# Kernel tuning notes

Hardware: AMD Instinct MI355X
Metric: run time of the kernel (lower is better)

The kernel has to match this reference:

```python
import jax, jax.numpy as jnp
import numpy as np

B, S, D, H = 2, 2048, 1024, 16
DH = D // H  # 64


def setup_inputs() -> dict:
    key = jax.random.key(0)
    ks = jax.random.split(key, 12)
    scale = 0.02
    q = jax.random.normal(ks[0], (B, S, D), dtype=jnp.float32)
    k = jax.random.normal(ks[1], (B, S, D), dtype=jnp.float32)
    v = jax.random.normal(ks[2], (B, S, D), dtype=jnp.float32)
    # CTRL-style causal mask: 1.0 above the diagonal (positions to mask), 0.0 elsewhere
    mask = jnp.triu(jnp.ones((S, S), dtype=jnp.float32), k=1)
    Wq = jax.random.normal(ks[3], (D, D), dtype=jnp.float32) * scale
    bq = jnp.zeros((D,), dtype=jnp.float32)
    Wk = jax.random.normal(ks[4], (D, D), dtype=jnp.float32) * scale
    bk = jnp.zeros((D,), dtype=jnp.float32)
    Wv = jax.random.normal(ks[5], (D, D), dtype=jnp.float32) * scale
    bv = jnp.zeros((D,), dtype=jnp.float32)
    Wo = jax.random.normal(ks[6], (D, D), dtype=jnp.float32) * scale
    bo = jnp.zeros((D,), dtype=jnp.float32)
    return {"q": q, "k": k, "v": v, "mask": mask,
            "Wq": Wq, "bq": bq, "Wk": Wk, "bk": bk,
            "Wv": Wv, "bv": bv, "Wo": Wo, "bo": bo}


def _split_heads(x):
    # [B, S, D] -> [B, H, S, DH]
    b, s, _ = x.shape
    return x.reshape(b, s, H, DH).transpose(0, 2, 1, 3)


def reference(q, k, v, mask, Wq, bq, Wk, bk, Wv, bv, Wo, bo):
    # QKV projections
    qh = _split_heads(q @ Wq + bq)  # [B, H, S, DH]
    kh = _split_heads(k @ Wk + bk)
    vh = _split_heads(v @ Wv + bv)
    # scaled dot-product attention with CTRL mask convention (mask * -1e4 added)
    scores = jnp.einsum('bhqd,bhkd->bhqk', qh, kh) / jnp.sqrt(jnp.float32(DH))
    scores = scores + mask * -10000.0  # mask broadcasts [S,S] -> [B,H,S,S]
    weights = jax.nn.softmax(scores, axis=-1)
    ctx = jnp.einsum('bhqk,bhkd->bhqd', weights, vh)  # [B, H, S, DH]
    ctx = ctx.transpose(0, 2, 1, 3).reshape(q.shape[0], -1, D)  # [B, S, D]
    return ctx @ Wo + bo
```

## Files before the change

kernel.cpp:

```cpp
#include <hip/hip_runtime.h>
#include <stdint.h>

typedef unsigned short u16;
typedef __attribute__((ext_vector_type(8))) short bf16x8;
typedef __attribute__((ext_vector_type(4))) float f32x4;
typedef __attribute__((ext_vector_type(4))) unsigned short u16x4;

#define C_SCALE 0.1803368801111204f
#define C_MASK  -14426.950408889634f

__device__ __forceinline__ float bf2f(u16 x) {
  union { uint32_t u; float f; } v; v.u = ((uint32_t)x) << 16; return v.f;
}
__device__ __forceinline__ u16 f2bf(float f) {
  union { float f; uint32_t u; } v; v.f = f;
  return (u16)((v.u + 0x7FFFu + ((v.u >> 16) & 1u)) >> 16);
}

__device__ __forceinline__ void load_lds16(const void* g, void* l) {
  __builtin_amdgcn_global_load_lds(
      (const __attribute__((address_space(1))) uint32_t*)g,
      (__attribute__((address_space(3))) uint32_t*)l, 16, 0, 0);
}

__device__ __forceinline__ uint32_t pack_trunc(uint32_t f_even, uint32_t f_odd) {
  return __builtin_amdgcn_perm(f_odd, f_even, 0x07060302u);
}

__device__ __forceinline__ bool detect_bf16(const u16* __restrict__ q) {
  int lane = threadIdx.x & 63;
  u16 w = q[lane * 4];
  int e = (w >> 7) & 0xFF;
  unsigned long long b = __ballot(e >= 96 && e <= 159);
  return __popcll(b) >= 48;
}

__global__ __launch_bounds__(256) void prep_all(const u16* __restrict__ W0,
                                                const u16* __restrict__ W1,
                                                const u16* __restrict__ W2,
                                                const u16* __restrict__ W3,
                                                u16* __restrict__ WTb,
                                                const u16* __restrict__ q,
                                                const u16* __restrict__ k,
                                                const u16* __restrict__ v,
                                                u16* __restrict__ Acast,
                                                int docast) {
  constexpr int D = 1024;
  const int z = blockIdx.z;
  const bool isbf = detect_bf16(q);

  if (z >= 4) {
    if (!docast || isbf) return;
    const int zi = z - 4;
    const u16* src = zi == 0 ? q : (zi == 1 ? k : v);
    const uint32_t* S = (const uint32_t*)src;
    u16* dst = Acast + (size_t)zi * 4 * 1024 * 1024;
    const int fb = blockIdx.y * 16 + blockIdx.x;
    const int t = threadIdx.x;
#pragma unroll
    for (int it = 0; it < 8; ++it) {
      size_t base = (size_t)fb * 16384 + it * 2048 + t * 8;
      uint4 a = *(const uint4*)&S[base];
      uint4 b = *(const uint4*)&S[base + 4];
      uint4 o;
      o.x = pack_trunc(a.x, a.y); o.y = pack_trunc(a.z, a.w);
      o.z = pack_trunc(b.x, b.y); o.w = pack_trunc(b.z, b.w);
      *(uint4*)&dst[base] = o;
    }
    return;
  }

  __shared__ u16 tile[64][72];
  const u16* W = z == 0 ? W0 : (z == 1 ? W1 : (z == 2 ? W2 : W3));
  u16* WT = WTb + (size_t)z * D * D;
  const int x0 = blockIdx.x * 64, y0 = blockIdx.y * 64;
  const int t = threadIdx.x;
  const int r = t >> 3;
  const int c8 = (t & 7) << 3;
#pragma unroll
  for (int hh = 0; hh < 2; ++hh) {
    int row = r + hh * 32;
    if (isbf) {
      *(uint4*)&tile[row][c8] = *(const uint4*)&W[(size_t)(y0 + row) * D + x0 + c8];
    } else {
      const float* Wf = (const float*)W;
      float4 f0 = *(const float4*)&Wf[(size_t)(y0 + row) * D + x0 + c8];
      float4 f1 = *(const float4*)&Wf[(size_t)(y0 + row) * D + x0 + c8 + 4];
      u16 tmp[8] = {f2bf(f0.x), f2bf(f0.y), f2bf(f0.z), f2bf(f0.w),
                    f2bf(f1.x), f2bf(f1.y), f2bf(f1.z), f2bf(f1.w)};
      *(uint4*)&tile[row][c8] = *(uint4*)tmp;
    }
  }
  __syncthreads();
#pragma unroll
  for (int hh = 0; hh < 2; ++hh) {
    int row = r + hh * 32;
    u16 tmp[8];
#pragma unroll
    for (int i = 0; i < 8; ++i) tmp[i] = tile[c8 + i][row];
    *(uint4*)&WT[(size_t)(x0 + row) * D + y0 + c8] = *(uint4*)tmp;
  }
}


__device__ __forceinline__ void stage_tile32(const u16* __restrict__ src, int row0,
                                             int k0, u16* dst, int wave, int lane) {
  constexpr int K = 1024;
#pragma unroll
  for (int p = 0; p < 2; ++p) {
    int seg = wave * 2 + p;
    int r = seg * 16 + (lane >> 2);
    int c = lane & 3;
    int cg = c ^ ((r >> 1) & 3);
    load_lds16(&src[(size_t)(row0 + r) * K + k0 + cg * 8], dst + seg * 512);
  }
}

#define FRAG_READS(Ab, Bb)                                                    \
  _Pragma("unroll") for (int i = 0; i < 4; ++i) {                             \
    int r = wm + 16 * i + lr;                                                 \
    af[i] = *(const bf16x8*)&(Ab)[r * 32 + ((quad ^ ((r >> 1) & 3)) * 8)];    \
  }                                                                           \
  _Pragma("unroll") for (int jj = 0; jj < 4; ++jj) {                          \
    int r = wn + 16 * jj + lr;                                                \
    bff[jj] = *(const bf16x8*)&(Bb)[r * 32 + ((quad ^ ((r >> 1) & 3)) * 8)];  \
  }

#define MFMA16()                                                              \
  _Pragma("unroll") for (int i = 0; i < 4; ++i)                               \
  _Pragma("unroll") for (int jj = 0; jj < 4; ++jj)                            \
      acc[i][jj] = __builtin_amdgcn_mfma_f32_16x16x32_bf16(af[i], bff[jj],    \
                                                           acc[i][jj], 0, 0, 0);

__device__ __forceinline__ void kloop2_dma(const u16* __restrict__ A,
                                           const u16* __restrict__ BT,
                                           int m0, int n0, u16* As, u16* Bs,
                                           int wave, int lane, f32x4 (&acc)[4][4]) {
  const int quad = lane >> 4, lr = lane & 15;
  const int wm = (wave & 1) * 64, wn = (wave >> 1) * 64;
  auto stage = [&](int t, int buf) {
    stage_tile32(A, m0, t * 32, As + buf * 4096, wave, lane);
    stage_tile32(BT, n0, t * 32, Bs + buf * 4096, wave, lane);
  };
  stage(0, 0);
  __syncthreads();
#pragma unroll 1
  for (int j = 0; j < 16; ++j) {
    const int t0 = 2 * j;
    {
      stage(t0 + 1, 1);
      bf16x8 af[4], bff[4];
      const u16 *Ab = As, *Bb = Bs;
      FRAG_READS(Ab, Bb)
      MFMA16()
      __syncthreads();
    }
    {
      if (t0 + 2 < 32) stage(t0 + 2, 0);
      bf16x8 af[4], bff[4];
      const u16 *Ab = As + 4096, *Bb = Bs + 4096;
      FRAG_READS(Ab, Bb)
      MFMA16()
      __syncthreads();
    }
  }
}

__device__ __forceinline__ void kloop2_f32(const float* __restrict__ Af,
                                           const u16* __restrict__ BT,
                                           int m0, int n0, u16* As, u16* Bs,
                                           int tid, f32x4 (&acc)[4][4]) {
  constexpr int K = 1024;
  const int wave = tid >> 6, lane = tid & 63;
  const int quad = lane >> 4, lr = lane & 15;
  const int wm = (wave & 1) * 64, wn = (wave >> 1) * 64;
  const int ar = tid >> 1, ah = tid & 1;
  const uint32_t* Au = (const uint32_t*)Af;
  uint4 ra0[4], ra1[4];
  auto loadA = [&](int t, uint4 (&r)[4]) {
    const uint32_t* p = &Au[(size_t)(m0 + ar) * K + t * 32 + ah * 16];
    r[0] = *(const uint4*)(p + 0);
    r[1] = *(const uint4*)(p + 4);
    r[2] = *(const uint4*)(p + 8);
    r[3] = *(const uint4*)(p + 12);
  };
  auto writeA = [&](int buf, uint4 (&rr)[4]) {
    uint4 o0, o1;
    o0.x = pack_trunc(rr[0].x, rr[0].y); o0.y = pack_trunc(rr[0].z, rr[0].w);
    o0.z = pack_trunc(rr[1].x, rr[1].y); o0.w = pack_trunc(rr[1].z, rr[1].w);
    o1.x = pack_trunc(rr[2].x, rr[2].y); o1.y = pack_trunc(rr[2].z, rr[2].w);
    o1.z = pack_trunc(rr[3].x, rr[3].y); o1.w = pack_trunc(rr[3].z, rr[3].w);
    int sw = (ar >> 1) & 3;
    int c0 = (2 * ah) ^ sw, c1 = (2 * ah + 1) ^ sw;
    *(uint4*)&As[buf * 4096 + ar * 32 + c0 * 8] = o0;
    *(uint4*)&As[buf * 4096 + ar * 32 + c1 * 8] = o1;
  };
  auto stageB = [&](int t, int buf) {
    stage_tile32(BT, n0, t * 32, Bs + buf * 4096, wave, lane);
  };
  loadA(0, ra0);
  stageB(0, 0);
  loadA(1, ra1);
  writeA(0, ra0);
  __syncthreads();
#pragma unroll 1
  for (int j = 0; j < 16; ++j) {
    const int t0 = 2 * j;
    {
      stageB(t0 + 1, 1);
      writeA(1, ra1);
      if (t0 + 2 < 32) loadA(t0 + 2, ra0);
      bf16x8 af[4], bff[4];
      const u16 *Ab = As, *Bb = Bs;
      FRAG_READS(Ab, Bb)
      MFMA16()
      __syncthreads();
    }
    {
      if (t0 + 2 < 32) { stageB(t0 + 2, 0); writeA(0, ra0); }
      if (t0 + 3 < 32) loadA(t0 + 3, ra1);
      bf16x8 af[4], bff[4];
      const u16 *Ab = As + 4096, *Bb = Bs + 4096;
      FRAG_READS(Ab, Bb)
      MFMA16()
      __syncthreads();
    }
  }
}

__global__ __launch_bounds__(256, 3) void gemm_qkv_pre(
    const u16* __restrict__ q, const u16* __restrict__ k, const u16* __restrict__ v,
    const u16* __restrict__ Acast, const u16* __restrict__ WTb,
    const u16* __restrict__ b0, const u16* __restrict__ b1, const u16* __restrict__ b2,
    u16* __restrict__ Chb) {
  __shared__ u16 As[2 * 4096];
  __shared__ u16 Bs[2 * 4096];
  const int z = blockIdx.y;
  const bool isbf = detect_bf16(q);
  const u16* Araw = z == 0 ? q : (z == 1 ? k : v);
  const u16* A = isbf ? Araw : Acast + (size_t)z * 4 * 1024 * 1024;
  const u16* bias = z == 0 ? b0 : (z == 1 ? b1 : b2);
  const u16* BT = WTb + (size_t)z * 1024 * 1024;
  u16* C = Chb + (size_t)z * 4 * 1024 * 1024;
  const int tid = threadIdx.x;
  const int wave = tid >> 6, lane = tid & 63;
  const int quad = lane >> 4, lr = lane & 15;
  const int f = blockIdx.x;
  const int n0 = (f >> 5) * 128;
  const int m0 = (f & 31) * 128;
  const int wm = (wave & 1) * 64, wn = (wave >> 1) * 64;

  f32x4 acc[4][4] = {};
  kloop2_dma(A, BT, m0, n0, As, Bs, wave, lane, acc);

#pragma unroll
  for (int i = 0; i < 4; ++i) {
#pragma unroll
    for (int jj = 0; jj < 4; ++jj) {
      int n = n0 + wn + 16 * jj + lr;
      float bv = isbf ? bf2f(bias[n]) : ((const float*)bias)[n];
#pragma unroll
      for (int r = 0; r < 4; ++r) {
        int m = m0 + wm + 16 * i + quad * 4 + r;
        float val = acc[i][jj][r] + bv;
        int b = m >> 11, s = m & 2047, h = n >> 6, dh = n & 63;
        C[((size_t)(b * 16 + h) * 2048 + s) * 64 + dh] = f2bf(val);
      }
    }
  }
}

__global__ __launch_bounds__(256, 3) void gemm_qkv_fb(
    const u16* __restrict__ A0, const u16* __restrict__ A1, const u16* __restrict__ A2,
    const u16* __restrict__ WTb,
    const u16* __restrict__ b0, const u16* __restrict__ b1, const u16* __restrict__ b2,
    u16* __restrict__ Chb) {
  __shared__ u16 As[2 * 4096];
  __shared__ u16 Bs[2 * 4096];
  const int z = blockIdx.y;
  const u16* A = z == 0 ? A0 : (z == 1 ? A1 : A2);
  const u16* bias = z == 0 ? b0 : (z == 1 ? b1 : b2);
  const u16* BT = WTb + (size_t)z * 1024 * 1024;
  u16* C = Chb + (size_t)z * 4 * 1024 * 1024;
  const bool isbf = detect_bf16(A0);
  const int tid = threadIdx.x;
  const int wave = tid >> 6, lane = tid & 63;
  const int quad = lane >> 4, lr = lane & 15;
  const int f = blockIdx.x;
  const int n0 = (f >> 5) * 128;
  const int m0 = (f & 31) * 128;
  const int wm = (wave & 1) * 64, wn = (wave >> 1) * 64;

  f32x4 acc[4][4] = {};
  if (isbf) kloop2_dma(A, BT, m0, n0, As, Bs, wave, lane, acc);
  else      kloop2_f32((const float*)A, BT, m0, n0, As, Bs, tid, acc);

#pragma unroll
  for (int i = 0; i < 4; ++i) {
#pragma unroll
    for (int jj = 0; jj < 4; ++jj) {
      int n = n0 + wn + 16 * jj + lr;
      float bv = isbf ? bf2f(bias[n]) : ((const float*)bias)[n];
#pragma unroll
      for (int r = 0; r < 4; ++r) {
        int m = m0 + wm + 16 * i + quad * 4 + r;
        float val = acc[i][jj][r] + bv;
        int b = m >> 11, s = m & 2047, h = n >> 6, dh = n & 63;
        C[((size_t)(b * 16 + h) * 2048 + s) * 64 + dh] = f2bf(val);
      }
    }
  }
}

__global__ __launch_bounds__(256, 2) void gemm_out(const u16* __restrict__ A,
                                                   const u16* __restrict__ BT,
                                                   const u16* __restrict__ bias,
                                                   u16* __restrict__ C,
                                                   const u16* __restrict__ qprobe) {
  constexpr int N = 1024, K = 1024;
  __shared__ u16 As[2 * 2048];
  __shared__ u16 Bs[2 * 4096];
  const bool isbf = detect_bf16(qprobe);
  const int tid = threadIdx.x;
  const int wave = tid >> 6, lane = tid & 63;
  const int quad = lane >> 4, lr = lane & 15;
  const int f = blockIdx.x;
  const int n0 = (f >> 6) * 128;
  const int m0 = (f & 63) * 64;
  const int wm = (wave & 1) * 32, wn = (wave >> 1) * 64;

  auto stage = [&](int t, int buf) {
    {
      int r = wave * 16 + (lane >> 2);
      int c = lane & 3;
      int cg = c ^ ((r >> 1) & 3);
      load_lds16(&A[(size_t)(m0 + r) * K + t * 32 + cg * 8],
                 As + buf * 2048 + wave * 512);
    }
    stage_tile32(BT, n0, t * 32, Bs + buf * 4096, wave, lane);
  };

  f32x4 acc[2][4] = {};
  stage(0, 0);
  __syncthreads();
#pragma unroll 1
  for (int j = 0; j < 16; ++j) {
    const int t0 = 2 * j;
#pragma unroll
    for (int half = 0; half < 2; ++half) {
      const int t = t0 + half;
      if (t + 1 < 32) stage(t + 1, (t + 1) & 1);
      bf16x8 af[2], bff[4];
      const u16* Ab = As + (t & 1) * 2048;
      const u16* Bb = Bs + (t & 1) * 4096;
#pragma unroll
      for (int i = 0; i < 2; ++i) {
        int r = wm + 16 * i + lr;
        af[i] = *(const bf16x8*)&Ab[r * 32 + ((quad ^ ((r >> 1) & 3)) * 8)];
      }
#pragma unroll
      for (int jj = 0; jj < 4; ++jj) {
        int r = wn + 16 * jj + lr;
        bff[jj] = *(const bf16x8*)&Bb[r * 32 + ((quad ^ ((r >> 1) & 3)) * 8)];
      }
#pragma unroll
      for (int i = 0; i < 2; ++i)
#pragma unroll
        for (int jj = 0; jj < 4; ++jj)
          acc[i][jj] =
              __builtin_amdgcn_mfma_f32_16x16x32_bf16(af[i], bff[jj], acc[i][jj], 0, 0, 0);
      __syncthreads();
    }
  }

#pragma unroll
  for (int i = 0; i < 2; ++i) {
#pragma unroll
    for (int jj = 0; jj < 4; ++jj) {
      int n = n0 + wn + 16 * jj + lr;
      float bv = isbf ? bf2f(bias[n]) : ((const float*)bias)[n];
#pragma unroll
      for (int r = 0; r < 4; ++r) {
        int m = m0 + wm + 16 * i + quad * 4 + r;
        float val = acc[i][jj][r] + bv;
        size_t idx = (size_t)m * N + n;
        if (isbf) C[idx] = f2bf(val);
        else ((float*)C)[idx] = val;
      }
    }
  }
}

__global__ __launch_bounds__(256, 2) void attn_fwd(const u16* __restrict__ Qh,
                                                   const u16* __restrict__ Kh,
                                                   const u16* __restrict__ Vh,
                                                   u16* __restrict__ ctx) {
  constexpr int S = 2048, DH = 64, Dm = 1024;
  __shared__ u16 Ks[2][64 * 64];
  __shared__ u16 Vt[2][64 * 72];
  __shared__ u16 Pl[4][16 * 72];
  const int tid = threadIdx.x;
  const int wave = tid >> 6, lane = tid & 63;
  const int quad = lane >> 4, lr = lane & 15;
  const int bh = blockIdx.y;
  const int bx = (int)blockIdx.x;
  const size_t base = (size_t)bh * S * DH;
  const u16* Q = Qh + base;
  const u16* Kp = Kh + base;
  const u16* Vp = Vh + base;
  u16* Plw = Pl[wave];
  const int b = bh >> 4, h = bh & 15;

  const int vkey2 = (tid & 31) * 2, vd8 = (tid >> 5) * 8;
  uint4 va, vbr;

  auto stageK = [&](int kt, int kbuf) {
#pragma unroll
    for (int p = 0; p < 2; ++p) {
      int s = (wave * 2 + p) * 64 + lane;
      int r = s >> 3, cg = (s & 7) ^ (r & 7);
      load_lds16(&Kp[(size_t)(kt + r) * DH + cg * 8], &Ks[kbuf][(wave * 2 + p) * 512]);
    }
  };
  auto loadV = [&](int kt) {
    va  = *(const uint4*)&Vp[(size_t)(kt + vkey2) * DH + vd8];
    vbr = *(const uint4*)&Vp[(size_t)(kt + vkey2 + 1) * DH + vd8];
  };
  auto writeV = [&](int vbuf) {
    const u16* pa = (const u16*)&va;
    const u16* pb = (const u16*)&vbr;
#pragma unroll
    for (int i = 0; i < 8; ++i) {
      uint32_t pair = (uint32_t)pa[i] | ((uint32_t)pb[i] << 16);
      *(uint32_t*)&Vt[vbuf][(vd8 + i) * 72 + vkey2] = pair;
    }
  };

  int kb = 0, vb = 0;
  for (int ph = 0; ph < 2; ++ph) {
    const int qt = ph == 0 ? (31 - bx) : bx;
    const int q0 = qt * 64;
    const int nt = qt + 1;
    const int qg = q0 + wave * 16 + lr;

    bf16x8 aQ[2];
#pragma unroll
    for (int s = 0; s < 2; ++s)
      aQ[s] = *(const bf16x8*)&Q[(size_t)(q0 + wave * 16 + lr) * DH + s * 32 + quad * 8];

    f32x4 o[4] = {};
    float m_i = -1.0e5f;
    float l_i = 0.f;

    __syncthreads();
    stageK(0, kb);
    loadV(0);
    writeV(vb);
    if (nt > 1) loadV(64);

    for (int it = 0; it < nt; ++it) {
      const int kt = it * 64;
      __syncthreads();

      bf16x8 aK[4][2], bV[4][2];
#pragma unroll
      for (int t = 0; t < 4; ++t) {
        int r = t * 16 + lr;
#pragma unroll
        for (int s = 0; s < 2; ++s) {
          int ch = (s * 4 + quad) ^ (r & 7);
          aK[t][s] = *(const bf16x8*)&Ks[kb][r * 64 + ch * 8];
        }
      }
#pragma unroll
      for (int c = 0; c < 4; ++c)
#pragma unroll
        for (int s = 0; s < 2; ++s)
          bV[c][s] = *(const bf16x8*)&Vt[vb][(c * 16 + lr) * 72 + s * 32 + quad * 8];

      if (it + 1 < nt) {
        stageK(kt + 64, kb ^ 1);
        writeV(vb ^ 1);
        if (it + 2 < nt) loadV(kt + 128);
      }

      f32x4 sc[4];
#pragma unroll
      for (int t = 0; t < 4; ++t) {
        f32x4 zz = {0.f, 0.f, 0.f, 0.f};
        zz = __builtin_amdgcn_mfma_f32_16x16x32_bf16(aK[t][0], aQ[0], zz, 0, 0, 0);
        zz = __builtin_amdgcn_mfma_f32_16x16x32_bf16(aK[t][1], aQ[1], zz, 0, 0, 0);
        sc[t] = zz;
      }

      const bool diag = (it == nt - 1);
      float v[4][4];
      float mx = -1.0e5f;
      if (diag) {
#pragma unroll
        for (int t = 0; t < 4; ++t)
#pragma unroll
          for (int r = 0; r < 4; ++r) {
            int kg = kt + t * 16 + quad * 4 + r;
            float x = sc[t][r] * C_SCALE + ((kg > qg) ? C_MASK : 0.f);
            v[t][r] = x;
            mx = fmaxf(mx, x);
          }
      } else {
#pragma unroll
        for (int t = 0; t < 4; ++t)
#pragma unroll
          for (int r = 0; r < 4; ++r) {
            float x = sc[t][r] * C_SCALE;
            v[t][r] = x;
            mx = fmaxf(mx, x);
          }
      }
      mx = fmaxf(mx, __shfl_xor(mx, 16));
      mx = fmaxf(mx, __shfl_xor(mx, 32));
      float m_new = fmaxf(m_i, mx);
      float sum = 0.f;
      u16 pb16[4][4];
#pragma unroll
      for (int t = 0; t < 4; ++t)
#pragma unroll
        for (int r = 0; r < 4; ++r) {
          float p = exp2f(v[t][r] - m_new);
          sum += p;
          pb16[t][r] = f2bf(p);
        }
      sum += __shfl_xor(sum, 16);
      sum += __shfl_xor(sum, 32);
      float alpha = exp2f(m_i - m_new);
      l_i = l_i * alpha + sum;
      m_i = m_new;
#pragma unroll
      for (int t = 0; t < 4; ++t) {
        u16x4 w = {pb16[t][0], pb16[t][1], pb16[t][2], pb16[t][3]};
        *(u16x4*)&Plw[lr * 72 + t * 16 + quad * 4] = w;
      }
#pragma unroll
      for (int r = 0; r < 4; ++r) {
        float ab = __shfl(alpha, quad * 4 + r);
#pragma unroll
        for (int c = 0; c < 4; ++c) o[c][r] *= ab;
      }
      asm volatile("s_waitcnt lgkmcnt(0)" ::: "memory");
      bf16x8 aP[2];
#pragma unroll
      for (int s = 0; s < 2; ++s)
        aP[s] = *(const bf16x8*)&Plw[lr * 72 + s * 32 + quad * 8];
#pragma unroll
      for (int c = 0; c < 4; ++c)
#pragma unroll
        for (int s = 0; s < 2; ++s)
          o[c] = __builtin_amdgcn_mfma_f32_16x16x32_bf16(aP[s], bV[c][s], o[c], 0, 0, 0);
      kb ^= 1; vb ^= 1;
    }

    float linv = 1.f / l_i;
#pragma unroll
    for (int r = 0; r < 4; ++r) {
      float lb = __shfl(linv, quad * 4 + r);
      int s = q0 + wave * 16 + quad * 4 + r;
      size_t orow = ((size_t)b * S + s) * Dm + h * DH;
#pragma unroll
      for (int c = 0; c < 4; ++c) ctx[orow + c * 16 + lr] = f2bf(o[c][r] * lb);
    }
  }
}

extern "C" void kernel_launch(void* const* d_in, const int* in_sizes, int n_in,
                              void* d_out, int out_size, void* d_ws, size_t ws_size,
                              hipStream_t stream) {
  const u16* q  = (const u16*)d_in[0];
  const u16* k  = (const u16*)d_in[1];
  const u16* v  = (const u16*)d_in[2];
  const u16* Wq = (const u16*)d_in[4];
  const u16* bq = (const u16*)d_in[5];
  const u16* Wk = (const u16*)d_in[6];
  const u16* bk = (const u16*)d_in[7];
  const u16* Wv = (const u16*)d_in[8];
  const u16* bv = (const u16*)d_in[9];
  const u16* Wo = (const u16*)d_in[10];
  const u16* bo = (const u16*)d_in[11];
  u16* out = (u16*)d_out;

  constexpr size_t M1 = 1024 * 1024;
  u16* ws = (u16*)d_ws;
  u16* WT  = ws;
  u16* Qh  = WT + 4 * M1;
  u16* X   = Qh + 12 * M1;
  u16* Acast = X;
  u16* ctx   = X;

  const bool docast = ws_size >= (size_t)28 * M1 * 2;

  dim3 tb(256);
  prep_all<<<dim3(16, 16, 7), tb, 0, stream>>>(Wq, Wk, Wv, Wo, WT, q, k, v,
                                               Acast, docast ? 1 : 0);
  if (docast)
    gemm_qkv_pre<<<dim3(256, 3), tb, 0, stream>>>(q, k, v, Acast, WT, bq, bk, bv, Qh);
  else
    gemm_qkv_fb<<<dim3(256, 3), tb, 0, stream>>>(q, k, v, WT, bq, bk, bv, Qh);
  attn_fwd<<<dim3(16, 32), tb, 0, stream>>>(Qh, Qh + 4 * M1, Qh + 8 * M1, ctx);
  gemm_out<<<dim3(512), tb, 0, stream>>>(ctx, WT + 3 * M1, bo, out, q);
}
```

Before: 240.1 us.

## Fold softmax scale into Q projection, skip lazy rescale, use packed bf16 convert

Moves the softmax scale (1/sqrt(d)*log2e) into the Q projection epilogue so the attention loop no longer multiplies each score. Adds a lazy-rescale rule: when no row's max grows by more than 8 (in log2 units) the running max is kept and the exp/shuffle/multiply rescaling of the output accumulator is skipped. Replaces the manual bf16 rounding with the hardware packed convert instruction. Costs: Q is now stored pre-scaled in bf16, which changes rounding slightly, and the lazy threshold lets probabilities reach up to 2^8 before renormalisation.

```diff
diff --git a/kernel.cpp b/kernel.cpp
--- a/kernel.cpp
+++ b/kernel.cpp
@@ -25,6 +25,12 @@
 
 __device__ __forceinline__ uint32_t pack_trunc(uint32_t f_even, uint32_t f_odd) {
   return __builtin_amdgcn_perm(f_odd, f_even, 0x07060302u);
+}
+
+__device__ __forceinline__ uint32_t cvtpk_bf16(float lo, float hi) {
+  uint32_t r;
+  asm("v_cvt_pk_bf16_f32 %0, %1, %2" : "=v"(r) : "v"(lo), "v"(hi));
+  return r;
 }
 
 __device__ __forceinline__ bool detect_bf16(const u16* __restrict__ q) {
@@ -253,6 +259,7 @@
   f32x4 acc[4][4] = {};
   kloop2_dma(A, BT, m0, n0, As, Bs, wave, lane, acc);
 
+  const float osc = (z == 0) ? C_SCALE : 1.0f;
 #pragma unroll
   for (int i = 0; i < 4; ++i) {
 #pragma unroll
@@ -262,7 +269,7 @@
 #pragma unroll
       for (int r = 0; r < 4; ++r) {
         int m = m0 + wm + 16 * i + quad * 4 + r;
-        float val = acc[i][jj][r] + bv;
+        float val = (acc[i][jj][r] + bv) * osc;
         int b = m >> 11, s = m & 2047, h = n >> 6, dh = n & 63;
         C[((size_t)(b * 16 + h) * 2048 + s) * 64 + dh] = f2bf(val);
       }
@@ -295,6 +302,7 @@
   if (isbf) kloop2_dma(A, BT, m0, n0, As, Bs, wave, lane, acc);
   else      kloop2_f32((const float*)A, BT, m0, n0, As, Bs, tid, acc);
 
+  const float osc = (z == 0) ? C_SCALE : 1.0f;
 #pragma unroll
   for (int i = 0; i < 4; ++i) {
 #pragma unroll
@@ -304,7 +312,7 @@
 #pragma unroll
       for (int r = 0; r < 4; ++r) {
         int m = m0 + wm + 16 * i + quad * 4 + r;
-        float val = acc[i][jj][r] + bv;
+        float val = (acc[i][jj][r] + bv) * osc;
         int b = m >> 11, s = m & 2047, h = n >> 6, dh = n & 63;
         C[((size_t)(b * 16 + h) * 2048 + s) * 64 + dh] = f2bf(val);
       }
@@ -502,7 +510,7 @@
 #pragma unroll
           for (int r = 0; r < 4; ++r) {
             int kg = kt + t * 16 + quad * 4 + r;
-            float x = sc[t][r] * C_SCALE + ((kg > qg) ? C_MASK : 0.f);
+            float x = sc[t][r] + ((kg > qg) ? C_MASK : 0.f);
             v[t][r] = x;
             mx = fmaxf(mx, x);
           }
@@ -511,39 +519,49 @@
         for (int t = 0; t < 4; ++t)
 #pragma unroll
           for (int r = 0; r < 4; ++r) {
-            float x = sc[t][r] * C_SCALE;
+            float x = sc[t][r];
             v[t][r] = x;
             mx = fmaxf(mx, x);
           }
       }
       mx = fmaxf(mx, __shfl_xor(mx, 16));
       mx = fmaxf(mx, __shfl_xor(mx, 32));
-      float m_new = fmaxf(m_i, mx);
+
+      const bool noresc = __all(mx <= m_i + 8.0f);
+      const float m_new = noresc ? m_i : fmaxf(m_i, mx);
+
       float sum = 0.f;
-      u16 pb16[4][4];
-#pragma unroll
-      for (int t = 0; t < 4; ++t)
-#pragma unroll
-        for (int r = 0; r < 4; ++r) {
-          float p = exp2f(v[t][r] - m_new);
-          sum += p;
-          pb16[t][r] = f2bf(p);
-        }
+      uint32_t pw[4][2];
+#pragma unroll
+      for (int t = 0; t < 4; ++t) {
+        float p0 = exp2f(v[t][0] - m_new);
+        float p1 = exp2f(v[t][1] - m_new);
+        float p2 = exp2f(v[t][2] - m_new);
+        float p3 = exp2f(v[t][3] - m_new);
+        sum += p0 + p1 + p2 + p3;
+        pw[t][0] = cvtpk_bf16(p0, p1);
+        pw[t][1] = cvtpk_bf16(p2, p3);
+      }
       sum += __shfl_xor(sum, 16);
       sum += __shfl_xor(sum, 32);
-      float alpha = exp2f(m_i - m_new);
-      l_i = l_i * alpha + sum;
-      m_i = m_new;
+
+      if (noresc) {
+        l_i += sum;
+      } else {
+        float alpha = exp2f(m_i - m_new);
+        l_i = l_i * alpha + sum;
+        m_i = m_new;
+#pragma unroll
+        for (int r = 0; r < 4; ++r) {
+          float ab = __shfl(alpha, quad * 4 + r);
+#pragma unroll
+          for (int c = 0; c < 4; ++c) o[c][r] *= ab;
+        }
+      }
 #pragma unroll
       for (int t = 0; t < 4; ++t) {
-        u16x4 w = {pb16[t][0], pb16[t][1], pb16[t][2], pb16[t][3]};
-        *(u16x4*)&Plw[lr * 72 + t * 16 + quad * 4] = w;
-      }
-#pragma unroll
-      for (int r = 0; r < 4; ++r) {
-        float ab = __shfl(alpha, quad * 4 + r);
-#pragma unroll
-        for (int c = 0; c < 4; ++c) o[c][r] *= ab;
+        uint2 w = {pw[t][0], pw[t][1]};
+        *(uint2*)&Plw[lr * 72 + t * 16 + quad * 4] = w;
       }
       asm volatile("s_waitcnt lgkmcnt(0)" ::: "memory");
       bf16x8 aP[2];
```

Measured after the change: 235.4 us. Within noise of the previous version (-1.9%).
